# Optimization experiments

Hardware: AMD Instinct MI355X
Metric: run time of the kernel (lower is better)

The kernel has to match this reference:

```python
import jax, jax.numpy as jnp
import numpy as np

MARGIN = 1.0
NUM_CLASSES = 64

def setup_inputs() -> dict:
    key = jax.random.key(0)
    k1, k2 = jax.random.split(key)
    embeddings = jax.random.normal(k1, (4096, 512), dtype=jnp.float32)
    labels = jax.random.randint(k2, (4096,), 0, NUM_CLASSES, dtype=jnp.int64)
    return {"embeddings": embeddings, "labels": labels}

def _pairwise_dist(x):
    # Euclidean cdist via GEMM: ||xi||^2 + ||xj||^2 - 2 xi.xj, with a
    # grad-safe sqrt (zero distance -> zero, no nan gradient).
    sq_norms = jnp.sum(x * x, axis=1)                      # [B]
    sq = sq_norms[:, None] + sq_norms[None, :] - 2.0 * (x @ x.T)
    sq = jnp.maximum(sq, 0.0)
    pos = sq > 0.0
    return jnp.where(pos, jnp.sqrt(jnp.where(pos, sq, 1.0)), 0.0)

def reference(embeddings, labels):
    B = embeddings.shape[0]
    # L2 normalize (normalize=True)
    emb = embeddings / jnp.maximum(
        jnp.linalg.norm(embeddings, axis=1, keepdims=True), 1e-12)
    dist = _pairwise_dist(emb)                             # [B, B]
    same = labels[:, None] == labels[None, :]              # [B, B]
    eye = jnp.eye(B, dtype=bool)
    pos_mask = same & ~eye
    neg_mask = ~same
    pos_cnt = jnp.sum(pos_mask, axis=1)                    # [B]
    neg_cnt = jnp.sum(neg_mask, axis=1)
    # hard_positive=False -> mean over positive distances
    pos_stat = jnp.sum(jnp.where(pos_mask, dist, 0.0), axis=1) / jnp.maximum(pos_cnt, 1)
    # hardest negative = masked min (infinity trick)
    neg_stat = jnp.min(jnp.where(neg_mask, dist, jnp.inf), axis=1)
    per_row = jnp.maximum(pos_stat - neg_stat + MARGIN, 0.0)
    valid = (pos_cnt > 0) & (neg_cnt > 0)
    n_valid = jnp.sum(valid)
    total = jnp.sum(jnp.where(valid, per_row, 0.0))
    # reduction='mean' over valid rows; 0.0 if none valid
    return jnp.where(n_valid > 0, total / jnp.maximum(n_valid, 1), 0.0)
```

## Files before the change

kernel.cpp:

```cpp
#include <hip/hip_runtime.h>
#include <hip/hip_bf16.h>

#define BSZ 4096
#define DIM 512
#define NCLS 64
#define MARGIN_F 1.0f
#define NT 32
#define NPAIR (NT * (NT + 1) / 2)
#define NSL (2 * NT)
#define NFIN 16
#define BK 64
#define NKS (DIM / BK)

typedef float floatx4 __attribute__((ext_vector_type(4)));
typedef unsigned char u8;

#define OFF_PP  (BSZ * DIM)
#define OFF_PN  (OFF_PP + NSL * BSZ * 4)
#define OFF_ACC (OFF_PN + NSL * BSZ * 4)

__device__ __forceinline__ void gld_lds16(const u8* g, u8* l) {
    __builtin_amdgcn_global_load_lds(
        (const __attribute__((address_space(1))) unsigned int*)g,
        (__attribute__((address_space(3))) unsigned int*)l, 16, 0, 0);
}

__global__ __launch_bounds__(256) void ht_normalize(
        const float* __restrict__ emb, u8* __restrict__ ebf,
        float* __restrict__ acc_total, int* __restrict__ acc_nv,
        int* __restrict__ counter2) {
    const int lane = threadIdx.x & 63;
    const int row = blockIdx.x * 4 + (threadIdx.x >> 6);
    const float4* r4 = (const float4*)(emb + (size_t)row * DIM);
    float4 v0 = r4[lane * 2];
    float4 v1 = r4[lane * 2 + 1];
    float s = v0.x * v0.x + v0.y * v0.y + v0.z * v0.z + v0.w * v0.w
            + v1.x * v1.x + v1.y * v1.y + v1.z * v1.z + v1.w * v1.w;
#pragma unroll
    for (int off = 1; off < 64; off <<= 1) s += __shfl_xor(s, off);
    const float inv = 1.0f / fmaxf(sqrtf(s), 1e-12f);

    int d0 = 0, d1 = 0;
    d0 = __builtin_amdgcn_cvt_pk_fp8_f32(v0.x * inv, v0.y * inv, d0, 0);
    d0 = __builtin_amdgcn_cvt_pk_fp8_f32(v0.z * inv, v0.w * inv, d0, 1);
    d1 = __builtin_amdgcn_cvt_pk_fp8_f32(v1.x * inv, v1.y * inv, d1, 0);
    d1 = __builtin_amdgcn_cvt_pk_fp8_f32(v1.z * inv, v1.w * inv, d1, 1);
    uint2 o; o.x = (unsigned)d0; o.y = (unsigned)d1;
    ((uint2*)(ebf + (size_t)row * DIM))[lane] = o;

    if (blockIdx.x == 0 && threadIdx.x == 0) {
        *acc_total = 0.0f; *acc_nv = 0; *counter2 = 0;
    }
}

__global__ __launch_bounds__(256, 4) void ht_gemm_reduce(
        const u8* __restrict__ ebf, const int* __restrict__ labels,
        float* __restrict__ part_ps, unsigned* __restrict__ part_nm) {
    __shared__ u8 sA[3][128 * BK];
    __shared__ u8 sB[3][128 * BK];
    __shared__ int sLI[128];
    __shared__ int sLJ[128];

    const int p = blockIdx.x;
    int rem = p, by = 0;
    while (rem >= NT - by) { rem -= NT - by; ++by; }
    const int bx = by + rem;
    const bool offd = (bx != by);

    const int t = threadIdx.x;
    const int row0 = by * 128;
    const int col0 = bx * 128;

    if (t < 128) sLI[t] = labels[row0 + t];
    else sLJ[t - 128] = labels[col0 + (t - 128)];

    const int lane = t & 63;
    const int wave = t >> 6;
    const int wr = (wave >> 1) * 64;
    const int wc = (wave & 1) * 64;
    const int l15 = lane & 15;
    const int quad = lane >> 4;

    const int gc = (t & 3) ^ ((t >> 3) & 3);
    const u8* gA0 = ebf + (size_t)(row0 + (t >> 2)) * DIM + gc * 16;
    const u8* gA1 = ebf + (size_t)(row0 + 64 + (t >> 2)) * DIM + gc * 16;
    const u8* gB0 = ebf + (size_t)(col0 + (t >> 2)) * DIM + gc * 16;
    const u8* gB1 = ebf + (size_t)(col0 + 64 + (t >> 2)) * DIM + gc * 16;
    const int lb0 = wave * 64 * 16;
    const int lb1 = (256 + wave * 64) * 16;

    floatx4 acc[4][4] = {};

    gld_lds16(gA0, &sA[0][lb0]);
    gld_lds16(gA1, &sA[0][lb1]);
    gld_lds16(gB0, &sB[0][lb0]);
    gld_lds16(gB1, &sB[0][lb1]);
    gld_lds16(gA0 + BK, &sA[1][lb0]);
    gld_lds16(gA1 + BK, &sA[1][lb1]);
    gld_lds16(gB0 + BK, &sB[1][lb0]);
    gld_lds16(gB1 + BK, &sB[1][lb1]);

#pragma unroll
    for (int ks = 0; ks < NKS; ++ks) {
        if (ks == 0)
            asm volatile("s_waitcnt vmcnt(4) lgkmcnt(0)" ::: "memory");
        else if (ks < NKS - 1)
            asm volatile("s_waitcnt vmcnt(4)" ::: "memory");
        else
            asm volatile("s_waitcnt vmcnt(0)" ::: "memory");
        __builtin_amdgcn_s_barrier();
        __builtin_amdgcn_sched_barrier(0);

        if (ks + 2 < NKS) {
            const int kb = (ks + 2) * BK;
            const int bn = (ks + 2) % 3;
            gld_lds16(gA0 + kb, &sA[bn][lb0]);
            gld_lds16(gA1 + kb, &sA[bn][lb1]);
            gld_lds16(gB0 + kb, &sB[bn][lb0]);
            gld_lds16(gB1 + kb, &sB[bn][lb1]);
        }
        const int bc = ks % 3;
#pragma unroll
        for (int h = 0; h < 2; ++h) {
            const int co = (((h * 2 + (quad >> 1)) ^ ((l15 >> 1) & 3)) * 16)
                         + (quad & 1) * 8;
            long af[4]; long bf[4];
#pragma unroll
            for (int mi = 0; mi < 4; ++mi)
                af[mi] = *(const long*)(&sA[bc][(wr + mi * 16 + l15) * BK + co]);
#pragma unroll
            for (int ni = 0; ni < 4; ++ni)
                bf[ni] = *(const long*)(&sB[bc][(wc + ni * 16 + l15) * BK + co]);
#pragma unroll
            for (int mi = 0; mi < 4; ++mi)
#pragma unroll
                for (int ni = 0; ni < 4; ++ni)
                    acc[mi][ni] = __builtin_amdgcn_mfma_f32_16x16x32_fp8_fp8(
                        af[mi], bf[ni], acc[mi][ni], 0, 0, 0);
        }
    }

    const float INF = __uint_as_float(0x7F800000u);
    const int rslice = 2 * bx + (wc >> 6);
    float psc[4] = {0.f, 0.f, 0.f, 0.f};
    float nmc[4] = {INF, INF, INF, INF};
#pragma unroll
    for (int mi = 0; mi < 4; ++mi) {
        const int rbase = wr + mi * 16 + quad * 4;
#pragma unroll
        for (int r = 0; r < 4; ++r) {
            const int rloc = rbase + r;
            const int gi = row0 + rloc;
            const int rl = sLI[rloc];
            float ps = 0.0f, nm = INF;
#pragma unroll
            for (int ni = 0; ni < 4; ++ni) {
                const int cloc = wc + ni * 16 + l15;
                const int gj = col0 + cloc;
                const int cl = sLJ[cloc];
                const float d = __builtin_amdgcn_sqrtf(
                    fmaxf(2.0f - 2.0f * acc[mi][ni][r], 0.0f));
                if (rl == cl) {
                    if (gi != gj) ps += d;
                    if (offd) psc[ni] += d;
                } else {
                    nm = fminf(nm, d);
                    if (offd) nmc[ni] = fminf(nmc[ni], d);
                }
            }
#pragma unroll
            for (int off = 1; off < 16; off <<= 1) {
                ps += __shfl_xor(ps, off);
                nm = fminf(nm, __shfl_xor(nm, off));
            }
            if (l15 == 0) {
                part_ps[rslice * BSZ + gi] = ps;
                part_nm[rslice * BSZ + gi] = __float_as_uint(nm);
            }
        }
    }
    if (offd) {
        const int cslice = 2 * by + (wr >> 6);
#pragma unroll
        for (int ni = 0; ni < 4; ++ni) {
            float ps = psc[ni], nm = nmc[ni];
            ps += __shfl_xor(ps, 16); ps += __shfl_xor(ps, 32);
            nm = fminf(nm, __shfl_xor(nm, 16));
            nm = fminf(nm, __shfl_xor(nm, 32));
            if (quad == 0) {
                const int gj = col0 + wc + ni * 16 + l15;
                part_ps[cslice * BSZ + gj] = ps;
                part_nm[cslice * BSZ + gj] = __float_as_uint(nm);
            }
        }
    }
}

__global__ __launch_bounds__(256) void ht_finalize(
        const float* __restrict__ part_ps, const unsigned* __restrict__ part_nm,
        const int* __restrict__ labels, float* __restrict__ acc_total,
        int* __restrict__ acc_nv, int* __restrict__ counter2,
        float* __restrict__ out) {
    __shared__ int hist[NCLS];
    __shared__ float sT[4];
    __shared__ int sN[4];
    const int t = threadIdx.x;
    if (t < NCLS) hist[t] = 0;
    __syncthreads();
    for (int i = t; i < BSZ; i += 256) atomicAdd(&hist[labels[i]], 1);
    __syncthreads();

    const int j = blockIdx.x * 256 + t;
    float ps = 0.0f;
    float nm = __uint_as_float(0x7F800000u);
#pragma unroll 8
    for (int s = 0; s < NSL; ++s) {
        ps += part_ps[s * BSZ + j];
        nm = fminf(nm, __uint_as_float(part_nm[s * BSZ + j]));
    }
    const int cnt = hist[labels[j]];
    const int pc = cnt - 1;
    const int nc = BSZ - cnt;
    float loss = 0.0f;
    int lv = 0;
    if (pc > 0 && nc > 0) {
        loss = fmaxf(ps / (float)pc - nm + MARGIN_F, 0.0f);
        lv = 1;
    }
#pragma unroll
    for (int off = 1; off < 64; off <<= 1) {
        loss += __shfl_xor(loss, off);
        lv += __shfl_xor(lv, off);
    }
    if ((t & 63) == 0) { sT[t >> 6] = loss; sN[t >> 6] = lv; }
    __syncthreads();
    if (t == 0) {
        const float tt = sT[0] + sT[1] + sT[2] + sT[3];
        const int nn = sN[0] + sN[1] + sN[2] + sN[3];
        __hip_atomic_fetch_add(acc_total, tt, __ATOMIC_ACQ_REL,
                               __HIP_MEMORY_SCOPE_AGENT);
        __hip_atomic_fetch_add(acc_nv, nn, __ATOMIC_ACQ_REL,
                               __HIP_MEMORY_SCOPE_AGENT);
        const int old2 = __hip_atomic_fetch_add(counter2, 1, __ATOMIC_ACQ_REL,
                                                __HIP_MEMORY_SCOPE_AGENT);
        if (old2 == NFIN - 1) {
            const float ft = __hip_atomic_load(acc_total, __ATOMIC_ACQUIRE,
                                               __HIP_MEMORY_SCOPE_AGENT);
            const int fn = __hip_atomic_load(acc_nv, __ATOMIC_ACQUIRE,
                                             __HIP_MEMORY_SCOPE_AGENT);
            out[0] = (fn > 0) ? ft / (float)fn : 0.0f;
        }
    }
}

extern "C" void kernel_launch(void* const* d_in, const int* in_sizes, int n_in,
                              void* d_out, int out_size, void* d_ws, size_t ws_size,
                              hipStream_t stream) {
    const float* emb = (const float*)d_in[0];
    const int* labels = (const int*)d_in[1];
    float* out = (float*)d_out;
    char* ws = (char*)d_ws;

    u8* ebf = (u8*)ws;
    float* part_ps = (float*)(ws + OFF_PP);
    unsigned* part_nm = (unsigned*)(ws + OFF_PN);
    float* acc_total = (float*)(ws + OFF_ACC);
    int* acc_nv = (int*)(ws + OFF_ACC + 4);
    int* counter2 = (int*)(ws + OFF_ACC + 8);

    ht_normalize<<<BSZ / 4, 256, 0, stream>>>(emb, ebf, acc_total, acc_nv,
                                              counter2);
    ht_gemm_reduce<<<NPAIR, 256, 0, stream>>>(ebf, labels, part_ps, part_nm);
    ht_finalize<<<NFIN, 256, 0, stream>>>(part_ps, part_nm, labels,
                                          acc_total, acc_nv, counter2, out);
}
```

Measured before the change: 86.97 us.

## Fuse finalize into GEMM kernel via last-blocks ticket and spin-wait

Removes the separate finalize kernel launch. Each GEMM block takes an atomic ticket when it finishes; the last NFIN blocks spin until all blocks are done and then perform the per-row reduction and loss accumulation. This saves one kernel launch and its gap in exchange for atomic stores and loads of the partials and a spin-wait that depends on those tail blocks being resident. Those blocks take tickets only after finishing their own tiles, so deadlock is unlikely.

```diff
diff --git a/kernel.cpp b/kernel.cpp
--- a/kernel.cpp
+++ b/kernel.cpp
@@ -28,7 +28,7 @@
 __global__ __launch_bounds__(256) void ht_normalize(
         const float* __restrict__ emb, u8* __restrict__ ebf,
         float* __restrict__ acc_total, int* __restrict__ acc_nv,
-        int* __restrict__ counter2) {
+        int* __restrict__ counter2, int* __restrict__ gemm_done) {
     const int lane = threadIdx.x & 63;
     const int row = blockIdx.x * 4 + (threadIdx.x >> 6);
     const float4* r4 = (const float4*)(emb + (size_t)row * DIM);
@@ -49,17 +49,24 @@
     ((uint2*)(ebf + (size_t)row * DIM))[lane] = o;
 
     if (blockIdx.x == 0 && threadIdx.x == 0) {
-        *acc_total = 0.0f; *acc_nv = 0; *counter2 = 0;
+        *acc_total = 0.0f; *acc_nv = 0; *counter2 = 0; *gemm_done = 0;
     }
 }
 
 __global__ __launch_bounds__(256, 4) void ht_gemm_reduce(
         const u8* __restrict__ ebf, const int* __restrict__ labels,
-        float* __restrict__ part_ps, unsigned* __restrict__ part_nm) {
+        float* __restrict__ part_ps, unsigned* __restrict__ part_nm,
+        float* __restrict__ acc_total, int* __restrict__ acc_nv,
+        int* __restrict__ counter2, int* __restrict__ gemm_done,
+        float* __restrict__ out) {
     __shared__ u8 sA[3][128 * BK];
     __shared__ u8 sB[3][128 * BK];
     __shared__ int sLI[128];
     __shared__ int sLJ[128];
+    __shared__ int sTicket;
+    __shared__ int hist[NCLS];
+    __shared__ float sT[4];
+    __shared__ int sN[4];
 
     const int p = blockIdx.x;
     int rem = p, by = 0;
@@ -174,8 +181,11 @@
                 nm = fminf(nm, __shfl_xor(nm, off));
             }
             if (l15 == 0) {
-                part_ps[rslice * BSZ + gi] = ps;
-                part_nm[rslice * BSZ + gi] = __float_as_uint(nm);
+                __hip_atomic_store(&part_ps[rslice * BSZ + gi], ps,
+                                   __ATOMIC_RELAXED, __HIP_MEMORY_SCOPE_AGENT);
+                __hip_atomic_store(&part_nm[rslice * BSZ + gi],
+                                   __float_as_uint(nm),
+                                   __ATOMIC_RELAXED, __HIP_MEMORY_SCOPE_AGENT);
             }
         }
     }
@@ -189,34 +199,45 @@
             nm = fminf(nm, __shfl_xor(nm, 32));
             if (quad == 0) {
                 const int gj = col0 + wc + ni * 16 + l15;
-                part_ps[cslice * BSZ + gj] = ps;
-                part_nm[cslice * BSZ + gj] = __float_as_uint(nm);
-            }
-        }
-    }
-}
-
-__global__ __launch_bounds__(256) void ht_finalize(
-        const float* __restrict__ part_ps, const unsigned* __restrict__ part_nm,
-        const int* __restrict__ labels, float* __restrict__ acc_total,
-        int* __restrict__ acc_nv, int* __restrict__ counter2,
-        float* __restrict__ out) {
-    __shared__ int hist[NCLS];
-    __shared__ float sT[4];
-    __shared__ int sN[4];
-    const int t = threadIdx.x;
+                __hip_atomic_store(&part_ps[cslice * BSZ + gj], ps,
+                                   __ATOMIC_RELAXED, __HIP_MEMORY_SCOPE_AGENT);
+                __hip_atomic_store(&part_nm[cslice * BSZ + gj],
+                                   __float_as_uint(nm),
+                                   __ATOMIC_RELAXED, __HIP_MEMORY_SCOPE_AGENT);
+            }
+        }
+    }
+
+    __syncthreads();
+    if (t == 0)
+        sTicket = __hip_atomic_fetch_add(gemm_done, 1, __ATOMIC_ACQ_REL,
+                                         __HIP_MEMORY_SCOPE_AGENT);
+    __syncthreads();
+    const int ticket = sTicket;
+    if (ticket < NPAIR - NFIN) return;
+    if (t == 0) {
+        while (__hip_atomic_load(gemm_done, __ATOMIC_ACQUIRE,
+                                 __HIP_MEMORY_SCOPE_AGENT) < NPAIR)
+            __builtin_amdgcn_s_sleep(2);
+    }
+    __syncthreads();
+
+    const int chunk = ticket - (NPAIR - NFIN);
     if (t < NCLS) hist[t] = 0;
     __syncthreads();
     for (int i = t; i < BSZ; i += 256) atomicAdd(&hist[labels[i]], 1);
     __syncthreads();
 
-    const int j = blockIdx.x * 256 + t;
+    const int j = chunk * 256 + t;
     float ps = 0.0f;
     float nm = __uint_as_float(0x7F800000u);
 #pragma unroll 8
     for (int s = 0; s < NSL; ++s) {
-        ps += part_ps[s * BSZ + j];
-        nm = fminf(nm, __uint_as_float(part_nm[s * BSZ + j]));
+        ps += __hip_atomic_load(&part_ps[s * BSZ + j], __ATOMIC_RELAXED,
+                                __HIP_MEMORY_SCOPE_AGENT);
+        nm = fminf(nm, __uint_as_float(
+                 __hip_atomic_load(&part_nm[s * BSZ + j], __ATOMIC_RELAXED,
+                                   __HIP_MEMORY_SCOPE_AGENT)));
     }
     const int cnt = hist[labels[j]];
     const int pc = cnt - 1;
@@ -267,10 +288,11 @@
     float* acc_total = (float*)(ws + OFF_ACC);
     int* acc_nv = (int*)(ws + OFF_ACC + 4);
     int* counter2 = (int*)(ws + OFF_ACC + 8);
+    int* gemm_done = (int*)(ws + OFF_ACC + 12);
 
     ht_normalize<<<BSZ / 4, 256, 0, stream>>>(emb, ebf, acc_total, acc_nv,
-                                              counter2);
-    ht_gemm_reduce<<<NPAIR, 256, 0, stream>>>(ebf, labels, part_ps, part_nm);
-    ht_finalize<<<NFIN, 256, 0, stream>>>(part_ps, part_nm, labels,
-                                          acc_total, acc_nv, counter2, out);
-}
+                                              counter2, gemm_done);
+    ht_gemm_reduce<<<NPAIR, 256, 0, stream>>>(ebf, labels, part_ps, part_nm,
+                                              acc_total, acc_nv, counter2,
+                                              gemm_done, out);
+}
```

New measurement: 89.59 us. +3.0%, slower.

## Fuse normalize, GEMM-reduce and finalize into one persistent kernel with grid barriers

Applied to the files above, without the earlier changes.

Merges the three launches into a single kernel of NPAIR=528 blocks. The first 512 blocks each normalize 8 rows, then every block waits on a global atomic barrier before running the GEMM tile. The last 16 blocks to finish, picked by ticket, spin until all tiles are done and then run the finalize. This removes two kernel launch gaps, at the cost of a memset, spin-wait barriers that need all 528 blocks resident at once (occupancy is dropped to 3 blocks per CU for this), and the risk of deadlock if they are not.

```diff
diff --git a/kernel.cpp b/kernel.cpp
--- a/kernel.cpp
+++ b/kernel.cpp
@@ -25,41 +25,58 @@
         (__attribute__((address_space(3))) unsigned int*)l, 16, 0, 0);
 }
 
-__global__ __launch_bounds__(256) void ht_normalize(
-        const float* __restrict__ emb, u8* __restrict__ ebf,
-        float* __restrict__ acc_total, int* __restrict__ acc_nv,
-        int* __restrict__ counter2) {
-    const int lane = threadIdx.x & 63;
-    const int row = blockIdx.x * 4 + (threadIdx.x >> 6);
-    const float4* r4 = (const float4*)(emb + (size_t)row * DIM);
-    float4 v0 = r4[lane * 2];
-    float4 v1 = r4[lane * 2 + 1];
-    float s = v0.x * v0.x + v0.y * v0.y + v0.z * v0.z + v0.w * v0.w
-            + v1.x * v1.x + v1.y * v1.y + v1.z * v1.z + v1.w * v1.w;
-#pragma unroll
-    for (int off = 1; off < 64; off <<= 1) s += __shfl_xor(s, off);
-    const float inv = 1.0f / fmaxf(sqrtf(s), 1e-12f);
-
-    int d0 = 0, d1 = 0;
-    d0 = __builtin_amdgcn_cvt_pk_fp8_f32(v0.x * inv, v0.y * inv, d0, 0);
-    d0 = __builtin_amdgcn_cvt_pk_fp8_f32(v0.z * inv, v0.w * inv, d0, 1);
-    d1 = __builtin_amdgcn_cvt_pk_fp8_f32(v1.x * inv, v1.y * inv, d1, 0);
-    d1 = __builtin_amdgcn_cvt_pk_fp8_f32(v1.z * inv, v1.w * inv, d1, 1);
-    uint2 o; o.x = (unsigned)d0; o.y = (unsigned)d1;
-    ((uint2*)(ebf + (size_t)row * DIM))[lane] = o;
-
-    if (blockIdx.x == 0 && threadIdx.x == 0) {
-        *acc_total = 0.0f; *acc_nv = 0; *counter2 = 0;
-    }
-}
-
-__global__ __launch_bounds__(256, 4) void ht_gemm_reduce(
-        const u8* __restrict__ ebf, const int* __restrict__ labels,
-        float* __restrict__ part_ps, unsigned* __restrict__ part_nm) {
+__global__ __launch_bounds__(256, 3) void ht_one(
+        const float* __restrict__ emb, const int* __restrict__ labels,
+        u8* __restrict__ ebf, float* __restrict__ part_ps,
+        unsigned* __restrict__ part_nm, float* __restrict__ acc_total,
+        int* __restrict__ acc_nv, int* __restrict__ counter2,
+        int* __restrict__ norm_done, int* __restrict__ gemm_done,
+        float* __restrict__ out) {
     __shared__ u8 sA[3][128 * BK];
     __shared__ u8 sB[3][128 * BK];
     __shared__ int sLI[128];
     __shared__ int sLJ[128];
+    __shared__ int sTicket;
+    __shared__ int hist[NCLS];
+    __shared__ float sT[4];
+    __shared__ int sN[4];
+
+    const int t = threadIdx.x;
+    const int lane = t & 63;
+    const int wave = t >> 6;
+
+    if (blockIdx.x < BSZ / 8) {
+#pragma unroll
+        for (int r = 0; r < 2; ++r) {
+            const int row = blockIdx.x * 8 + wave * 2 + r;
+            const float4* r4 = (const float4*)(emb + (size_t)row * DIM);
+            float4 v0 = r4[lane * 2];
+            float4 v1 = r4[lane * 2 + 1];
+            float s = v0.x * v0.x + v0.y * v0.y + v0.z * v0.z + v0.w * v0.w
+                    + v1.x * v1.x + v1.y * v1.y + v1.z * v1.z + v1.w * v1.w;
+#pragma unroll
+            for (int off = 1; off < 64; off <<= 1) s += __shfl_xor(s, off);
+            const float inv = 1.0f / fmaxf(sqrtf(s), 1e-12f);
+            int d0 = 0, d1 = 0;
+            d0 = __builtin_amdgcn_cvt_pk_fp8_f32(v0.x * inv, v0.y * inv, d0, 0);
+            d0 = __builtin_amdgcn_cvt_pk_fp8_f32(v0.z * inv, v0.w * inv, d0, 1);
+            d1 = __builtin_amdgcn_cvt_pk_fp8_f32(v1.x * inv, v1.y * inv, d1, 0);
+            d1 = __builtin_amdgcn_cvt_pk_fp8_f32(v1.z * inv, v1.w * inv, d1, 1);
+            uint2 o; o.x = (unsigned)d0; o.y = (unsigned)d1;
+            ((uint2*)(ebf + (size_t)row * DIM))[lane] = o;
+        }
+    }
+
+    __syncthreads();
+    if (t == 0) {
+        __hip_atomic_fetch_add(norm_done, 1, __ATOMIC_RELEASE,
+                               __HIP_MEMORY_SCOPE_AGENT);
+        while (__hip_atomic_load(norm_done, __ATOMIC_RELAXED,
+                                 __HIP_MEMORY_SCOPE_AGENT) < NPAIR)
+            __builtin_amdgcn_s_sleep(16);
+        __threadfence();
+    }
+    __syncthreads();
 
     const int p = blockIdx.x;
     int rem = p, by = 0;
@@ -67,15 +84,12 @@
     const int bx = by + rem;
     const bool offd = (bx != by);
 
-    const int t = threadIdx.x;
     const int row0 = by * 128;
     const int col0 = bx * 128;
 
     if (t < 128) sLI[t] = labels[row0 + t];
     else sLJ[t - 128] = labels[col0 + (t - 128)];
 
-    const int lane = t & 63;
-    const int wave = t >> 6;
     const int wr = (wave >> 1) * 64;
     const int wc = (wave & 1) * 64;
     const int l15 = lane & 15;
@@ -194,23 +208,29 @@
             }
         }
     }
-}
-
-__global__ __launch_bounds__(256) void ht_finalize(
-        const float* __restrict__ part_ps, const unsigned* __restrict__ part_nm,
-        const int* __restrict__ labels, float* __restrict__ acc_total,
-        int* __restrict__ acc_nv, int* __restrict__ counter2,
-        float* __restrict__ out) {
-    __shared__ int hist[NCLS];
-    __shared__ float sT[4];
-    __shared__ int sN[4];
-    const int t = threadIdx.x;
+
+    __syncthreads();
+    if (t == 0)
+        sTicket = __hip_atomic_fetch_add(gemm_done, 1, __ATOMIC_RELEASE,
+                                         __HIP_MEMORY_SCOPE_AGENT);
+    __syncthreads();
+    const int ticket = sTicket;
+    if (ticket < NPAIR - NFIN) return;
+    if (t == 0) {
+        while (__hip_atomic_load(gemm_done, __ATOMIC_RELAXED,
+                                 __HIP_MEMORY_SCOPE_AGENT) < NPAIR)
+            __builtin_amdgcn_s_sleep(16);
+        __threadfence();
+    }
+    __syncthreads();
+
+    const int chunk = ticket - (NPAIR - NFIN);
     if (t < NCLS) hist[t] = 0;
     __syncthreads();
     for (int i = t; i < BSZ; i += 256) atomicAdd(&hist[labels[i]], 1);
     __syncthreads();
 
-    const int j = blockIdx.x * 256 + t;
+    const int j = chunk * 256 + t;
     float ps = 0.0f;
     float nm = __uint_as_float(0x7F800000u);
 #pragma unroll 8
@@ -267,10 +287,11 @@
     float* acc_total = (float*)(ws + OFF_ACC);
     int* acc_nv = (int*)(ws + OFF_ACC + 4);
     int* counter2 = (int*)(ws + OFF_ACC + 8);
-
-    ht_normalize<<<BSZ / 4, 256, 0, stream>>>(emb, ebf, acc_total, acc_nv,
-                                              counter2);
-    ht_gemm_reduce<<<NPAIR, 256, 0, stream>>>(ebf, labels, part_ps, part_nm);
-    ht_finalize<<<NFIN, 256, 0, stream>>>(part_ps, part_nm, labels,
-                                          acc_total, acc_nv, counter2, out);
+    int* norm_done = (int*)(ws + OFF_ACC + 12);
+    int* gemm_done = (int*)(ws + OFF_ACC + 16);
+
+    hipMemsetAsync(ws + OFF_ACC, 0, 32, stream);
+    ht_one<<<NPAIR, 256, 0, stream>>>(emb, labels, ebf, part_ps, part_nm,
+                                      acc_total, acc_nv, counter2,
+                                      norm_done, gemm_done, out);
 }
```

Measured after the change: 135.0 us. +55.2%, slower.
